# Performance work log

Hardware: AMD Instinct MI355X
Metric: run time of the kernel (lower is better)

## Reference

```python
import jax, jax.numpy as jnp
import numpy as np
import math

N, D, H = 4096, 2048, 16
HD = D // H  # head_dim = 128


def setup_inputs() -> dict:
    key = jax.random.key(0)
    ks = jax.random.split(key, 9)
    s = 1.0 / math.sqrt(D)
    return {
        "x":  jax.random.normal(ks[0], (N, D), dtype=jnp.float32),
        "Wq": jax.random.normal(ks[1], (D, D), dtype=jnp.float32) * s,
        "bq": jax.random.normal(ks[2], (D,), dtype=jnp.float32) * s,
        "Wk": jax.random.normal(ks[3], (D, D), dtype=jnp.float32) * s,
        "bk": jax.random.normal(ks[4], (D,), dtype=jnp.float32) * s,
        "Wv": jax.random.normal(ks[5], (D, D), dtype=jnp.float32) * s,
        "bv": jax.random.normal(ks[6], (D,), dtype=jnp.float32) * s,
        "Wo": jax.random.normal(ks[7], (D, D), dtype=jnp.float32) * s,
        "bo": jax.random.normal(ks[8], (D,), dtype=jnp.float32) * s,
    }


def reference(x, Wq, bq, Wk, bk, Wv, bv, Wo, bo):
    # eqx.nn.Linear: y = W @ x + b, weight shape (out, in) -> x @ W.T + b
    q = x @ Wq.T + bq            # [N, D]
    k = x @ Wk.T + bk            # [N, D]
    v = x @ Wv.T + bv            # [N, D]
    q = q.reshape(N, H, HD).transpose(1, 0, 2)   # [H, N, hd]
    k = k.reshape(N, H, HD).transpose(1, 2, 0)   # [H, hd, N]
    v = v.reshape(N, H, HD).transpose(1, 0, 2)   # [H, N, hd]
    scale = 1.0 / math.sqrt(HD)
    scores = jnp.matmul(q * scale, k)            # [H, N, N]
    attn = jax.nn.softmax(scores, axis=-1)
    ctx = jnp.matmul(attn, v)                    # [H, N, hd]
    ctx = ctx.transpose(1, 0, 2).reshape(N, D)   # [N, D]
    return ctx @ Wo.T + bo
```

## Files before the change

kernel.cpp:

```cpp
#include <hip/hip_runtime.h>
#include <stdint.h>

#define N_TOK 4096
#define DIM   2048
#define NH    16
#define HD    128
#define NW    (DIM * DIM)

using bf16x8 = __attribute__((ext_vector_type(8))) short;
using bf16x4 = __attribute__((ext_vector_type(4))) short;
using f32x4  = __attribute__((ext_vector_type(4))) float;
using u32x2  = __attribute__((ext_vector_type(2))) unsigned int;

#if __has_builtin(__builtin_amdgcn_exp2f)
#define EXP2(x) __builtin_amdgcn_exp2f(x)
#else
#define EXP2(x) exp2f(x)
#endif

__device__ inline unsigned short f2bf(float f) {
  union { float f; unsigned u; } v; v.f = f;
  unsigned r = v.u + 0x7FFFu + ((v.u >> 16) & 1u);
  return (unsigned short)(r >> 16);
}
__device__ inline float bf2f(unsigned short u) {
  union { unsigned u; float f; } v; v.u = ((unsigned)u) << 16; return v.f;
}
__device__ inline f32x4 mfma16(bf16x8 a, bf16x8 b, f32x4 c) {
  return __builtin_amdgcn_mfma_f32_16x16x32_bf16(a, b, c, 0, 0, 0);
}
__device__ inline void gll16(const unsigned short* g, unsigned short* l) {
  __builtin_amdgcn_global_load_lds(
      (const __attribute__((address_space(1))) void*)g,
      (__attribute__((address_space(3))) void*)l, 16, 0, 0);
}

__device__ inline unsigned cvtpk_bf16(float lo, float hi) {
  unsigned r;
  asm("v_cvt_pk_bf16_f32 %0, %1, %2" : "=v"(r) : "v"(lo), "v"(hi));
  return r;
}

__device__ inline u32x2 pl32swap(unsigned a, unsigned b) {
#if __has_builtin(__builtin_amdgcn_permlane32_swap)
  return __builtin_amdgcn_permlane32_swap(a, b, false, false);
#else
  int lane = threadIdx.x & 63;
  unsigned as = (unsigned)__shfl_xor((int)a, 32);
  unsigned bs = (unsigned)__shfl_xor((int)b, 32);
  u32x2 r;
  r.x = (lane & 32) ? bs : a;
  r.y = (lane & 32) ? b : as;
  return r;
#endif
}
__device__ inline u32x2 pl16swap(unsigned a, unsigned b) {
#if __has_builtin(__builtin_amdgcn_permlane16_swap)
  return __builtin_amdgcn_permlane16_swap(a, b, false, false);
#else
  int lane = threadIdx.x & 63;
  unsigned as = (unsigned)__shfl_xor((int)a, 16);
  unsigned bs = (unsigned)__shfl_xor((int)b, 16);
  u32x2 r;
  r.x = (lane & 16) ? bs : a;
  r.y = (lane & 16) ? b : as;
  return r;
#endif
}

__global__ __launch_bounds__(256)
void cvt_bf16(const float* __restrict__ src, unsigned short* __restrict__ dst, int n) {
  int i = blockIdx.x * 256 + threadIdx.x;
  if (i * 8 >= n) return;
  const float4* s = (const float4*)src + (size_t)i * 2;
  float4 a = s[0], b = s[1];
  bf16x8 o;
  o[0] = (short)f2bf(a.x); o[1] = (short)f2bf(a.y);
  o[2] = (short)f2bf(a.z); o[3] = (short)f2bf(a.w);
  o[4] = (short)f2bf(b.x); o[5] = (short)f2bf(b.y);
  o[6] = (short)f2bf(b.z); o[7] = (short)f2bf(b.w);
  *(bf16x8*)(dst + (size_t)i * 8) = o;
}

template<int OUT_MODE>
__global__ __launch_bounds__(256)
void gemm_bf16(const unsigned short* __restrict__ A, const unsigned short* __restrict__ B,
               const float* __restrict__ bias, void* __restrict__ out_, float scale) {
  __shared__ unsigned short Asl[128 * 32];
  __shared__ unsigned short Bsl[128 * 32];
  const int tid  = threadIdx.x;
  const int lane = tid & 63, w = tid >> 6;
  const int wy = w >> 1, wx = w & 1;
  const int lr = lane & 15, quad = lane >> 4;
  const int m0 = blockIdx.y * 128, n0 = blockIdx.x * 128;

  const f32x4 vzero = {0.f, 0.f, 0.f, 0.f};
  f32x4 acc[4][4];
#pragma unroll
  for (int i = 0; i < 4; ++i)
#pragma unroll
    for (int j = 0; j < 4; ++j) acc[i][j] = vzero;

  for (int k0 = 0; k0 < DIM; k0 += 32) {
    __syncthreads();
#pragma unroll
    for (int i = 0; i < 2; ++i) {
      int ch = tid + i * 256;
      int r = ch >> 2, cc = ch & 3;
      gll16(&A[(size_t)(m0 + r) * DIM + k0 + cc * 8], &Asl[ch * 8]);
      gll16(&B[(size_t)(n0 + r) * DIM + k0 + cc * 8], &Bsl[ch * 8]);
    }
    __syncthreads();

    bf16x8 af[4], bfv[4];
#pragma unroll
    for (int mb = 0; mb < 4; ++mb)
      af[mb] = *(const bf16x8*)&Asl[(wy * 64 + mb * 16 + lr) * 32 + quad * 8];
#pragma unroll
    for (int nb = 0; nb < 4; ++nb)
      bfv[nb] = *(const bf16x8*)&Bsl[(wx * 64 + nb * 16 + lr) * 32 + quad * 8];
#pragma unroll
    for (int mb = 0; mb < 4; ++mb)
#pragma unroll
      for (int nb = 0; nb < 4; ++nb)
        acc[mb][nb] = mfma16(af[mb], bfv[nb], acc[mb][nb]);
  }

#pragma unroll
  for (int mb = 0; mb < 4; ++mb)
#pragma unroll
    for (int nb = 0; nb < 4; ++nb) {
      int gn = n0 + wx * 64 + nb * 16 + lr;
      int gm_base = m0 + wy * 64 + mb * 16 + quad * 4;
      float bs = bias[gn];
      if constexpr (OUT_MODE == 2) {
        bf16x4 pk;
#pragma unroll
        for (int r = 0; r < 4; ++r) pk[r] = (short)f2bf((acc[mb][nb][r] + bs) * scale);
        *(bf16x4*)&((unsigned short*)out_)[(size_t)gn * N_TOK + gm_base] = pk;
      } else {
#pragma unroll
        for (int r = 0; r < 4; ++r) {
          float v = (acc[mb][nb][r] + bs) * scale;
          if constexpr (OUT_MODE == 1)
            ((float*)out_)[(size_t)(gm_base + r) * DIM + gn] = v;
          else
            ((unsigned short*)out_)[(size_t)(gm_base + r) * DIM + gn] = f2bf(v);
        }
      }
    }
}

__global__ __launch_bounds__(256)
void flash_attn(const unsigned short* __restrict__ Q,
                const unsigned short* __restrict__ K,
                const unsigned short* __restrict__ Vt,
                unsigned short* __restrict__ ctx) {
  constexpr int LDK = 136;
  constexpr int LDV = 72;
  __shared__ unsigned short Ksl[64 * LDK];
  __shared__ unsigned short VTsl[128 * LDV];

  const int tid  = threadIdx.x;
  const int lane = tid & 63, w = tid >> 6;
  const int lr = lane & 15, quad = lane >> 4;
  const int hoff = blockIdx.y * HD;
  const int q0   = blockIdx.x * 128;
  const int qw   = q0 + w * 32;

  bf16x8 qf[2][4];
#pragma unroll
  for (int mb = 0; mb < 2; ++mb)
#pragma unroll
    for (int c = 0; c < 4; ++c)
      qf[mb][c] = *(const bf16x8*)&Q[(size_t)(qw + mb * 16 + lr) * DIM + hoff + c * 32 + quad * 8];

  const f32x4 vzero = {0.f, 0.f, 0.f, 0.f};
  f32x4 o[2][8];
  float l_acc[2] = {0.f, 0.f};
#pragma unroll
  for (int mb = 0; mb < 2; ++mb)
#pragma unroll
    for (int nb = 0; nb < 8; ++nb) o[mb][nb] = vzero;

  bf16x8 kreg[4], vreg[4];
  auto load_tile = [&](int kt) {
    int kbase = kt * 64;
#pragma unroll
    for (int i = 0; i < 4; ++i) {
      int ch = tid + i * 256;
      kreg[i] = *(const bf16x8*)&K[(size_t)(kbase + (ch >> 4)) * DIM + hoff + (ch & 15) * 8];
      vreg[i] = *(const bf16x8*)&Vt[(size_t)(hoff + (ch >> 3)) * N_TOK + kbase + (ch & 7) * 8];
    }
  };
  load_tile(0);

  for (int kt = 0; kt < N_TOK / 64; ++kt) {
    __syncthreads();
#pragma unroll
    for (int i = 0; i < 4; ++i) {
      int ch = tid + i * 256;
      *(bf16x8*)&Ksl[(ch >> 4) * LDK + (ch & 15) * 8] = kreg[i];
      *(bf16x8*)&VTsl[(ch >> 3) * LDV + (ch & 7) * 8] = vreg[i];
    }
    __syncthreads();
    if (kt + 1 < N_TOK / 64) load_tile(kt + 1);

    f32x4 s[2][4];
#pragma unroll
    for (int mb = 0; mb < 2; ++mb)
#pragma unroll
      for (int nf = 0; nf < 4; ++nf) s[mb][nf] = vzero;
#pragma unroll
    for (int nf = 0; nf < 4; ++nf)
#pragma unroll
      for (int c = 0; c < 4; ++c) {
        bf16x8 kf = *(const bf16x8*)&Ksl[(nf * 16 + lr) * LDK + c * 32 + quad * 8];
#pragma unroll
        for (int mb = 0; mb < 2; ++mb) s[mb][nf] = mfma16(kf, qf[mb][c], s[mb][nf]);
      }

    bf16x8 pf[2][2];
#pragma unroll
    for (int mb = 0; mb < 2; ++mb) {
      unsigned W[4][2];
      float lp = 0.f;
#pragma unroll
      for (int nf = 0; nf < 4; ++nf) {
        float e0 = EXP2(s[mb][nf][0]);
        float e1 = EXP2(s[mb][nf][1]);
        float e2 = EXP2(s[mb][nf][2]);
        float e3 = EXP2(s[mb][nf][3]);
        lp += (e0 + e1) + (e2 + e3);
        W[nf][0] = cvtpk_bf16(e0, e1);
        W[nf][1] = cvtpk_bf16(e2, e3);
      }
      l_acc[mb] += lp;
#pragma unroll
      for (int ki = 0; ki < 2; ++ki) {
        u32x2 a0  = pl32swap(W[2 * ki][0], W[2 * ki + 1][0]);
        u32x2 t02 = pl16swap(a0.x, a0.y);
        u32x2 a1  = pl32swap(W[2 * ki][1], W[2 * ki + 1][1]);
        u32x2 t13 = pl16swap(a1.x, a1.y);
        union { unsigned u[4]; bf16x8 v; } pu;
        pu.u[0] = t02.x; pu.u[1] = t13.x; pu.u[2] = t02.y; pu.u[3] = t13.y;
        pf[mb][ki] = pu.v;
      }
    }

#pragma unroll
    for (int nb = 0; nb < 8; ++nb)
#pragma unroll
      for (int ki = 0; ki < 2; ++ki) {
        bf16x8 vf = *(const bf16x8*)&VTsl[(nb * 16 + lr) * LDV + ki * 32 + quad * 8];
#pragma unroll
        for (int mb = 0; mb < 2; ++mb) o[mb][nb] = mfma16(pf[mb][ki], vf, o[mb][nb]);
      }
  }

#pragma unroll
  for (int mb = 0; mb < 2; ++mb) {
    float t = l_acc[mb];
    t += __shfl_xor(t, 16);
    t += __shfl_xor(t, 32);
    l_acc[mb] = t;
  }
#pragma unroll
  for (int mb = 0; mb < 2; ++mb)
#pragma unroll
    for (int r = 0; r < 4; ++r) {
      float Lr = __shfl(l_acc[mb], quad * 4 + r);
      float inv = 1.0f / Lr;
      int gq = qw + mb * 16 + quad * 4 + r;
#pragma unroll
      for (int nb = 0; nb < 8; ++nb)
        ctx[(size_t)gq * DIM + hoff + nb * 16 + lr] = f2bf(o[mb][nb][r] * inv);
    }
}

extern "C" void kernel_launch(void* const* d_in, const int* in_sizes, int n_in,
                              void* d_out, int out_size, void* d_ws, size_t ws_size,
                              hipStream_t stream) {
  (void)in_sizes; (void)n_in; (void)out_size; (void)ws_size;
  const float* x  = (const float*)d_in[0];
  const float* Wq = (const float*)d_in[1];
  const float* bq = (const float*)d_in[2];
  const float* Wk = (const float*)d_in[3];
  const float* bk = (const float*)d_in[4];
  const float* Wv = (const float*)d_in[5];
  const float* bv = (const float*)d_in[6];
  const float* Wo = (const float*)d_in[7];
  const float* bo = (const float*)d_in[8];

  const size_t NE = (size_t)N_TOK * DIM;
  unsigned short* xb  = (unsigned short*)d_ws;
  unsigned short* Wqb = xb + NE;
  unsigned short* Wkb = Wqb + NW;
  unsigned short* Wvb = Wkb + NW;
  unsigned short* Wob = Wvb + NW;
  unsigned short* Qb  = Wob + NW;
  unsigned short* Kb  = Qb + NE;
  unsigned short* Vtb = Kb + NE;

  cvt_bf16<<<4096, 256, 0, stream>>>(x,  xb,  (int)NE);
  cvt_bf16<<<2048, 256, 0, stream>>>(Wq, Wqb, NW);
  cvt_bf16<<<2048, 256, 0, stream>>>(Wk, Wkb, NW);
  cvt_bf16<<<2048, 256, 0, stream>>>(Wv, Wvb, NW);
  cvt_bf16<<<2048, 256, 0, stream>>>(Wo, Wob, NW);

  dim3 gemm_grid(DIM / 128, N_TOK / 128);
  const float qscale = 1.4426950408889634f * 0.08838834764831845f;

  gemm_bf16<0><<<gemm_grid, 256, 0, stream>>>(xb, Wqb, bq, Qb, qscale);
  gemm_bf16<0><<<gemm_grid, 256, 0, stream>>>(xb, Wkb, bk, Kb, 1.0f);
  gemm_bf16<2><<<gemm_grid, 256, 0, stream>>>(xb, Wvb, bv, Vtb, 1.0f);

  unsigned short* ctxb = xb;
  flash_attn<<<dim3(N_TOK / 128, NH), 256, 0, stream>>>(Qb, Kb, Vtb, ctxb);

  gemm_bf16<1><<<gemm_grid, 256, 0, stream>>>(ctxb, Wob, bo, (float*)d_out, 1.0f);
}
```

Baseline: 491.6 us.

## Software-pipeline flash attention so PV of previous tile overlaps softmax

Restructures the attention inner loop so the P·V MFMAs for tile kt-1 are issued together with the QK MFMAs for tile kt, and the exp/softmax of tile kt runs afterward. V^T is double-buffered in LDS so the previous tile's values stay valid while the next is staged. s_setprio raises wave priority around the MFMA block so matrix and exp work from different waves can interleave. This adds LDS usage and register pressure (s and pf live across iterations), which may reduce occupancy.

```diff
diff --git a/kernel.cpp b/kernel.cpp
--- a/kernel.cpp
+++ b/kernel.cpp
@@ -158,8 +158,9 @@
                 unsigned short* __restrict__ ctx) {
   constexpr int LDK = 136;
   constexpr int LDV = 72;
+  constexpr int NT  = N_TOK / 64;
   __shared__ unsigned short Ksl[64 * LDK];
-  __shared__ unsigned short VTsl[128 * LDV];
+  __shared__ unsigned short VTsl[2][128 * LDV];
 
   const int tid  = threadIdx.x;
   const int lane = tid & 63, w = tid >> 6;
@@ -193,20 +194,19 @@
       vreg[i] = *(const bf16x8*)&Vt[(size_t)(hoff + (ch >> 3)) * N_TOK + kbase + (ch & 7) * 8];
     }
   };
-  load_tile(0);
-
-  for (int kt = 0; kt < N_TOK / 64; ++kt) {
-    __syncthreads();
+  auto stage = [&](int buf) {
 #pragma unroll
     for (int i = 0; i < 4; ++i) {
       int ch = tid + i * 256;
       *(bf16x8*)&Ksl[(ch >> 4) * LDK + (ch & 15) * 8] = kreg[i];
-      *(bf16x8*)&VTsl[(ch >> 3) * LDV + (ch & 7) * 8] = vreg[i];
-    }
-    __syncthreads();
-    if (kt + 1 < N_TOK / 64) load_tile(kt + 1);
-
-    f32x4 s[2][4];
+      *(bf16x8*)&VTsl[buf][(ch >> 3) * LDV + (ch & 7) * 8] = vreg[i];
+    }
+  };
+
+  f32x4 s[2][4];
+  bf16x8 pf[2][2];
+
+  auto qk = [&]() {
 #pragma unroll
     for (int mb = 0; mb < 2; ++mb)
 #pragma unroll
@@ -219,8 +219,20 @@
 #pragma unroll
         for (int mb = 0; mb < 2; ++mb) s[mb][nf] = mfma16(kf, qf[mb][c], s[mb][nf]);
       }
-
-    bf16x8 pf[2][2];
+  };
+
+  auto pv = [&](int buf) {
+#pragma unroll
+    for (int nb = 0; nb < 8; ++nb)
+#pragma unroll
+      for (int ki = 0; ki < 2; ++ki) {
+        bf16x8 vf = *(const bf16x8*)&VTsl[buf][(nb * 16 + lr) * LDV + ki * 32 + quad * 8];
+#pragma unroll
+        for (int mb = 0; mb < 2; ++mb) o[mb][nb] = mfma16(pf[mb][ki], vf, o[mb][nb]);
+      }
+  };
+
+  auto softmax = [&]() {
 #pragma unroll
     for (int mb = 0; mb < 2; ++mb) {
       unsigned W[4][2];
@@ -247,16 +259,27 @@
         pf[mb][ki] = pu.v;
       }
     }
-
-#pragma unroll
-    for (int nb = 0; nb < 8; ++nb)
-#pragma unroll
-      for (int ki = 0; ki < 2; ++ki) {
-        bf16x8 vf = *(const bf16x8*)&VTsl[(nb * 16 + lr) * LDV + ki * 32 + quad * 8];
-#pragma unroll
-        for (int mb = 0; mb < 2; ++mb) o[mb][nb] = mfma16(pf[mb][ki], vf, o[mb][nb]);
-      }
+  };
+
+  load_tile(0);
+  stage(0);
+  __syncthreads();
+  load_tile(1);
+  qk();
+  softmax();
+
+  for (int kt = 1; kt < NT; ++kt) {
+    __syncthreads();
+    stage(kt & 1);
+    __syncthreads();
+    if (kt + 1 < NT) load_tile(kt + 1);
+    __builtin_amdgcn_s_setprio(1);
+    qk();
+    pv((kt - 1) & 1);
+    __builtin_amdgcn_s_setprio(0);
+    softmax();
   }
+  pv((NT - 1) & 1);
 
 #pragma unroll
   for (int mb = 0; mb < 2; ++mb) {
```

Result: slower. 541.2 us (+10.1%).
